# Kernel optimization log

Measured on AMD Instinct MI355X. Metric: run time of the kernel, lower is better.

## Reference

```python
import jax, jax.numpy as jnp
import numpy as np

S, IN, OUT = 2048, 512, 512
H, KV = 16, 4            # query heads, kv heads (cross-broadcast + averaged)
DQ = DK = DV = 64        # per-head embedding dims


def setup_inputs() -> dict:
    key = jax.random.key(0)
    ks = jax.random.split(key, 5)
    lim_in = 1.0 / np.sqrt(IN)
    lim_o = 1.0 / np.sqrt(H * DV)
    x = jax.random.normal(ks[0], (S, IN), dtype=jnp.float32)
    Wq = jax.random.uniform(ks[1], (H * DQ, IN), jnp.float32, -lim_in, lim_in)
    Wk = jax.random.uniform(ks[2], (KV * DK, IN), jnp.float32, -lim_in, lim_in)
    Wv = jax.random.uniform(ks[3], (KV * DV, IN), jnp.float32, -lim_in, lim_in)
    Wo = jax.random.uniform(ks[4], (OUT, H * DV), jnp.float32, -lim_o, lim_o)
    return {"x": x, "Wq": Wq, "Wk": Wk, "Wv": Wv, "Wo": Wo}


def reference(x, Wq, Wk, Wv, Wo):
    seq = x.shape[0]
    # projections (eqx.nn.Linear: y = W @ x, no bias)
    q = (x @ Wq.T).reshape(seq, H, DQ)    # [S, H, DQ]
    k = (x @ Wk.T).reshape(seq, KV, DK)   # [S, KV, DK]
    v = (x @ Wv.T).reshape(seq, KV, DV)   # [S, KV, DV]
    # cross-broadcast every kv head against every query head -> [KV, H, S, S]
    scores = jnp.einsum('shd,tkd->khst', q, k) / jnp.sqrt(jnp.asarray(DK, x.dtype))
    # NOTE: original applies causal mask whenever `mask is not None`; the
    # boolean flag is always passed, so masking is effectively always on.
    causal = jnp.tril(jnp.ones((seq, seq), dtype=bool))
    scores = jnp.where(causal, scores, -jnp.inf)
    w = jax.nn.softmax(scores, axis=-1)   # [KV, H, S, S]
    # attn @ V, then sum over kv heads and average by KV
    o = jnp.einsum('khst,tkd->shd', w, v) / KV  # [S, H, DV]
    return o.reshape(seq, H * DV) @ Wo.T        # [S, OUT]
```

## Files before the change

### kernel.cpp

```cpp
#include <hip/hip_runtime.h>
#include <hip/hip_bf16.h>

#define SEQ   2048
#define INF_  512
#define HQ    16
#define KVH   4
#define DH    64
#define NQ    (HQ*DH)
#define NKV   (KVH*DH)
#define OUTD  512

typedef short v8s __attribute__((ext_vector_type(8)));
typedef float v4f __attribute__((ext_vector_type(4)));

static __device__ __forceinline__ float bf2f(unsigned short u) {
    union { unsigned int i; float f; } c;
    c.i = ((unsigned int)u) << 16;
    return c.f;
}
static __device__ __forceinline__ unsigned short f2bf(float f) {
    union { float f; unsigned int i; } c; c.f = f;
    unsigned int lsb = (c.i >> 16) & 1u;
    c.i += 0x7fffu + lsb;
    return (unsigned short)(c.i >> 16);
}
static __device__ __forceinline__ unsigned int f2bf2(float lo, float hi) {
    union { __hip_bfloat162 h; unsigned int u; } c;
    c.h = __float22bfloat162_rn(make_float2(lo, hi));
    return c.u;
}
static __device__ __forceinline__ v8s pack8(v4f a, v4f b) {
    union { v8s s; uint4 u; } c;
    c.u = make_uint4(f2bf2(a[0], a[1]), f2bf2(a[2], a[3]),
                     f2bf2(b[0], b[1]), f2bf2(b[2], b[3]));
    return c.s;
}

static __device__ __forceinline__ void gll16(const void* g, void* l) {
    __builtin_amdgcn_global_load_lds(
        (const __attribute__((address_space(1))) void*)g,
        (__attribute__((address_space(3))) void*)l, 16, 0, 0);
}

static __device__ __forceinline__ void stage_tile(
    const unsigned short* __restrict__ src, int stride, int kb,
    unsigned short* ldsbase, int w, int lane)
{
#pragma unroll
    for (int i = 0; i < 2; i++) {
        const int rl = w * 16 + i * 8 + (lane >> 3);
        const int kc = ((lane & 7) ^ (rl & 7)) * 8;
        gll16(src + (size_t)rl * stride + kb + kc,
              ldsbase + (w * 16 + i * 8) * 64);
    }
}

#define QSCALE 0.180336880f

__global__ __launch_bounds__(256) void cast_all(
    const float* __restrict__ x,  const float* __restrict__ Wq,
    const float* __restrict__ Wk, const float* __restrict__ Wv,
    const float* __restrict__ Wo,
    unsigned short* __restrict__ xb,  unsigned short* __restrict__ Wqb,
    unsigned short* __restrict__ Wkb, unsigned short* __restrict__ Wvb,
    unsigned short* __restrict__ Wob)
{
    size_t i = ((size_t)blockIdx.x * 256 + threadIdx.x) * 8;
    const float* s; unsigned short* d; size_t off;
    if (i < 1048576)      { s = x;  d = xb;  off = i; }
    else if (i < 1572864) { s = Wq; d = Wqb; off = i - 1048576; }
    else if (i < 1703936) { s = Wk; d = Wkb; off = i - 1572864; }
    else if (i < 1835008) { s = Wv; d = Wvb; off = i - 1703936; }
    else                  { s = Wo; d = Wob; off = i - 1835008; }
    float4 a = *(const float4*)(s + off);
    float4 b = *(const float4*)(s + off + 4);
    *(uint4*)(d + off) = make_uint4(f2bf2(a.x, a.y), f2bf2(a.z, a.w),
                                    f2bf2(b.x, b.y), f2bf2(b.z, b.w));
}

__global__ __launch_bounds__(256, 4) void gemm_qkv(
    const unsigned short* __restrict__ xb,
    const unsigned short* __restrict__ Wqb,
    const unsigned short* __restrict__ Wkb,
    const unsigned short* __restrict__ Wvb,
    unsigned short* __restrict__ Qg,
    unsigned short* __restrict__ Kg,
    unsigned short* __restrict__ Vg)
{
    __shared__ unsigned short Asb[2][4096];
    __shared__ unsigned short Bsb[2][4096];

    const int m0 = blockIdx.x * 64;
    const int n0 = blockIdx.y * 64;

    const unsigned short* Bp; int role;
    if (n0 < NQ)            { Bp = Wqb + (size_t)n0 * INF_;              role = 0; }
    else if (n0 < NQ + NKV) { Bp = Wkb + (size_t)(n0 - NQ) * INF_;       role = 1; }
    else                    { Bp = Wvb + (size_t)(n0 - NQ - NKV) * INF_; role = 2; }

    const int tid = threadIdx.x;
    const int w = tid >> 6, lane = tid & 63;
    const int n = lane & 15, quad = lane >> 4;
    const int m7 = n & 7;
    const int r0w = (w & 1) * 32, c0w = (w >> 1) * 32;
    const unsigned short* Ap = xb + (size_t)m0 * INF_;

    v4f acc[2][2];
#pragma unroll
    for (int rt = 0; rt < 2; rt++)
#pragma unroll
        for (int ct = 0; ct < 2; ct++) acc[rt][ct] = (v4f){0.f,0.f,0.f,0.f};

    stage_tile(Ap, INF_, 0, &Asb[0][0], w, lane);
    stage_tile(Bp, INF_, 0, &Bsb[0][0], w, lane);

    for (int kb = 0; kb < INF_; kb += 64) {
        const int buf = (kb >> 6) & 1;
        __syncthreads();
        if (kb + 64 < INF_) {
            stage_tile(Ap, INF_, kb + 64, &Asb[buf ^ 1][0], w, lane);
            stage_tile(Bp, INF_, kb + 64, &Bsb[buf ^ 1][0], w, lane);
        }
#pragma unroll
        for (int kk = 0; kk < 2; kk++) {
            const int gs = ((kk * 4 + quad) ^ m7) * 8;
            v8s a0 = *(const v8s*)&Asb[buf][(r0w + n) * 64 + gs];
            v8s a1 = *(const v8s*)&Asb[buf][(r0w + 16 + n) * 64 + gs];
            v8s b0 = *(const v8s*)&Bsb[buf][(c0w + n) * 64 + gs];
            v8s b1 = *(const v8s*)&Bsb[buf][(c0w + 16 + n) * 64 + gs];
            acc[0][0] = __builtin_amdgcn_mfma_f32_16x16x32_bf16(a0, b0, acc[0][0], 0, 0, 0);
            acc[0][1] = __builtin_amdgcn_mfma_f32_16x16x32_bf16(a0, b1, acc[0][1], 0, 0, 0);
            acc[1][0] = __builtin_amdgcn_mfma_f32_16x16x32_bf16(a1, b0, acc[1][0], 0, 0, 0);
            acc[1][1] = __builtin_amdgcn_mfma_f32_16x16x32_bf16(a1, b1, acc[1][1], 0, 0, 0);
        }
    }

    const int t = m0 >> 6;
    if (role == 0) {
        unsigned short* base = Qg + ((size_t)(t * 16 + (n0 >> 6))) * 4096;
#pragma unroll
        for (int rt = 0; rt < 2; rt++)
#pragma unroll
            for (int ct = 0; ct < 2; ct++)
#pragma unroll
                for (int reg = 0; reg < 4; reg++) {
                    const int r = r0w + rt * 16 + quad * 4 + reg;
                    const int d = c0w + ct * 16 + n;
                    base[r * 64 + (((d >> 3) ^ (r & 7)) * 8) + (d & 7)] =
                        f2bf(acc[rt][ct][reg] * QSCALE);
                }
    } else if (role == 1) {
        const int g = (n0 - NQ) >> 6;
        unsigned short* base = Kg + ((size_t)(g * 32 + t)) * 4096;
#pragma unroll
        for (int rt = 0; rt < 2; rt++)
#pragma unroll
            for (int ct = 0; ct < 2; ct++)
#pragma unroll
                for (int reg = 0; reg < 4; reg++) {
                    const int r = r0w + rt * 16 + quad * 4 + reg;
                    const int d = c0w + ct * 16 + n;
                    base[r * 64 + (((d >> 3) ^ (r & 7)) * 8) + (d & 7)] =
                        f2bf(acc[rt][ct][reg]);
                }
    } else {
        const int g = (n0 - NQ - NKV) >> 6;
        unsigned short* base = Vg + ((size_t)(g * 32 + t)) * 4096;
#pragma unroll
        for (int rt = 0; rt < 2; rt++)
#pragma unroll
            for (int ct = 0; ct < 2; ct++) {
                const int jb_ = r0w + rt * 16 + quad * 4;
                const int d = c0w + ct * 16 + n;
                const int p = (jb_ & 32) + (((jb_ >> 2) & 3) * 8) + (((jb_ >> 4) & 1) * 4);
                *(uint2*)&base[d * 64 + (((p >> 3) ^ (d & 7)) * 8) + (p & 7)] =
                    make_uint2(f2bf2(acc[rt][ct][0], acc[rt][ct][1]),
                               f2bf2(acc[rt][ct][2], acc[rt][ct][3]));
            }
    }
}

__global__ __launch_bounds__(256, 4) void attn_mfma(
    const unsigned short* __restrict__ Qg,
    const unsigned short* __restrict__ Kg,
    const unsigned short* __restrict__ Vg,
    unsigned short* __restrict__ Oh)
{
    __shared__ unsigned short Ksb[2][4096];
    __shared__ unsigned short Vsb[2][4096];

    const int bx = blockIdx.x;
    const int h  = bx & 15;
    const int jj = (bx >> 4) & 15;
    const int g  = bx >> 8;
    const int jj2 = (jj + 8 * (g >> 1)) & 15;
    const int qi2 = (g & 1) ? (15 - jj2) : jj2;
    const int q0 = qi2 * 128;
    const int tid = threadIdx.x;
    const int w = tid >> 6, lane = tid & 63;
    const int n = lane & 15, quad = lane >> 4;
    const int r0 = w * 32;
    const int m7 = n & 7;
    const int ntile = 2 * qi2 + 2;

    {
        const size_t off = ((size_t)(g * 32)) * 4096 + w * 1024 + lane * 8;
        gll16(Kg + off,       &Ksb[0][w * 1024]);
        gll16(Kg + off + 512, &Ksb[0][w * 1024 + 512]);
        gll16(Vg + off,       &Vsb[0][w * 1024]);
        gll16(Vg + off + 512, &Vsb[0][w * 1024 + 512]);
    }

    v8s qf[2][2];
    {
        const unsigned short* tb =
            Qg + ((size_t)((2 * qi2 + (r0 >> 6)) * 16 + h)) * 4096 + (r0 & 63) * 64;
#pragma unroll
        for (int qt = 0; qt < 2; qt++) {
            const unsigned short* rp = tb + (qt * 16 + n) * 64;
            qf[qt][0] = *(const v8s*)(rp + (quad ^ m7) * 8);
            qf[qt][1] = *(const v8s*)(rp + ((quad + 4) ^ m7) * 8);
        }
    }

    v8s ones;
#pragma unroll
    for (int i = 0; i < 8; i++) ones[i] = (short)0x3F80;

    v4f Lacc[2];
    Lacc[0] = (v4f){0.f,0.f,0.f,0.f};
    Lacc[1] = (v4f){0.f,0.f,0.f,0.f};
    v4f Oacc[2][4];
#pragma unroll
    for (int qt = 0; qt < 2; qt++)
#pragma unroll
        for (int dt = 0; dt < 4; dt++) Oacc[qt][dt] = (v4f){0.f,0.f,0.f,0.f};
    const v4f z = (v4f){0.f,0.f,0.f,0.f};

    for (int tt = 0; tt < ntile; tt++) {
        const int buf = tt & 1;
        __syncthreads();
        if (tt + 1 < ntile) {
            const size_t off = ((size_t)(g * 32 + tt + 1)) * 4096 + w * 1024 + lane * 8;
            const int nb = buf ^ 1;
            gll16(Kg + off,       &Ksb[nb][w * 1024]);
            gll16(Kg + off + 512, &Ksb[nb][w * 1024 + 512]);
            gll16(Vg + off,       &Vsb[nb][w * 1024]);
            gll16(Vg + off + 512, &Vsb[nb][w * 1024 + 512]);
        }
        const int t0 = tt * 64;
        const bool do0 = (t0 <= q0 + r0 + 15);
        const bool do1 = (t0 <= q0 + r0 + 31);
        if (!do1) continue;

        const unsigned short* Kb = Ksb[buf];
        const unsigned short* Vb = Vsb[buf];

        v4f sc[2][4];
#pragma unroll
        for (int jt = 0; jt < 4; jt++) {
            const int kr = (jt * 16 + n) * 64;
            v8s kf0 = *(const v8s*)&Kb[kr + (quad ^ m7) * 8];
            v8s kf1 = *(const v8s*)&Kb[kr + ((quad + 4) ^ m7) * 8];
            if (do0) {
                v4f tq = __builtin_amdgcn_mfma_f32_16x16x32_bf16(kf0, qf[0][0], z, 0, 0, 0);
                sc[0][jt] = __builtin_amdgcn_mfma_f32_16x16x32_bf16(kf1, qf[0][1], tq, 0, 0, 0);
            }
            v4f t1 = __builtin_amdgcn_mfma_f32_16x16x32_bf16(kf0, qf[1][0], z, 0, 0, 0);
            sc[1][jt] = __builtin_amdgcn_mfma_f32_16x16x32_bf16(kf1, qf[1][1], t1, 0, 0, 0);
        }

#pragma unroll
        for (int qt = 0; qt < 2; qt++) {
            if (qt == 0 && !do0) continue;
            const int qg = q0 + r0 + qt * 16 + n;
            if (t0 + 63 > q0 + r0 + qt * 16) {
#pragma unroll
                for (int jt = 0; jt < 4; jt++) {
                    const int jg = t0 + jt * 16 + quad * 4;
#pragma unroll
                    for (int reg = 0; reg < 4; reg++)
                        sc[qt][jt][reg] = (jg + reg <= qg) ? sc[qt][jt][reg] : -INFINITY;
                }
            }
#pragma unroll
            for (int jt = 0; jt < 4; jt++)
#pragma unroll
                for (int reg = 0; reg < 4; reg++)
                    sc[qt][jt][reg] = __builtin_amdgcn_exp2f(sc[qt][jt][reg]);
        }

        v8s pf[2][2];
        if (do0) {
            pf[0][0] = pack8(sc[0][0], sc[0][1]);
            pf[0][1] = pack8(sc[0][2], sc[0][3]);
        }
        pf[1][0] = pack8(sc[1][0], sc[1][1]);
        pf[1][1] = pack8(sc[1][2], sc[1][3]);

        if (do0) {
            Lacc[0] = __builtin_amdgcn_mfma_f32_16x16x32_bf16(ones, pf[0][0], Lacc[0], 0, 0, 0);
            Lacc[0] = __builtin_amdgcn_mfma_f32_16x16x32_bf16(ones, pf[0][1], Lacc[0], 0, 0, 0);
        }
        Lacc[1] = __builtin_amdgcn_mfma_f32_16x16x32_bf16(ones, pf[1][0], Lacc[1], 0, 0, 0);
        Lacc[1] = __builtin_amdgcn_mfma_f32_16x16x32_bf16(ones, pf[1][1], Lacc[1], 0, 0, 0);

#pragma unroll
        for (int dt = 0; dt < 4; dt++) {
            const int vr = (dt * 16 + n) * 64;
            v8s vf0 = *(const v8s*)&Vb[vr + (quad ^ m7) * 8];
            v8s vf1 = *(const v8s*)&Vb[vr + ((quad + 4) ^ m7) * 8];
            if (do0) {
                Oacc[0][dt] = __builtin_amdgcn_mfma_f32_16x16x32_bf16(vf0, pf[0][0], Oacc[0][dt], 0, 0, 0);
                Oacc[0][dt] = __builtin_amdgcn_mfma_f32_16x16x32_bf16(vf1, pf[0][1], Oacc[0][dt], 0, 0, 0);
            }
            Oacc[1][dt] = __builtin_amdgcn_mfma_f32_16x16x32_bf16(vf0, pf[1][0], Oacc[1][dt], 0, 0, 0);
            Oacc[1][dt] = __builtin_amdgcn_mfma_f32_16x16x32_bf16(vf1, pf[1][1], Oacc[1][dt], 0, 0, 0);
        }
    }

    unsigned short* Ohp = Oh + (size_t)g * ((size_t)SEQ * NQ);
#pragma unroll
    for (int qt = 0; qt < 2; qt++) {
        const float inv = 0.25f / Lacc[qt][0];
        const int row = q0 + r0 + qt * 16 + n;
        unsigned short* dst = Ohp + (size_t)row * NQ + h * DH + quad * 4;
#pragma unroll
        for (int dt = 0; dt < 4; dt++) {
            uint2 pk = make_uint2(f2bf2(Oacc[qt][dt][0] * inv, Oacc[qt][dt][1] * inv),
                                  f2bf2(Oacc[qt][dt][2] * inv, Oacc[qt][dt][3] * inv));
            *(uint2*)(dst + dt * 16) = pk;
        }
    }
}

__global__ __launch_bounds__(256, 4) void gemm_out(
    const unsigned short* __restrict__ Oh,
    const unsigned short* __restrict__ Wob,
    float* __restrict__ C)
{
    __shared__ unsigned short Asb[32][72];
    __shared__ unsigned short Bsb[64][72];

    const int m0 = blockIdx.x * 32;
    const int n0 = blockIdx.y * 64;
    const int tid = threadIdx.x;
    const int w = tid >> 6, lane = tid & 63;
    const int n = lane & 15, quad = lane >> 4;
    const int rw = (w & 1) * 16, cw = (w >> 1) * 32;
    const int ar = tid >> 3, akc = (tid & 7) * 8;
    const int br = tid >> 2, bkc = (tid & 3) * 16;

    v4f acc[2];
    acc[0] = (v4f){0.f,0.f,0.f,0.f};
    acc[1] = (v4f){0.f,0.f,0.f,0.f};

    const size_t plane = (size_t)SEQ * NQ;
    const size_t abase = (size_t)(m0 + ar) * NQ + akc;
    const unsigned short* bp = Wob + (size_t)(n0 + br) * NQ + bkc;

    uint4 ua[4];
#pragma unroll
    for (int g = 0; g < 4; g++) ua[g] = *(const uint4*)(Oh + g * plane + abase);
    uint4 ub0 = *(const uint4*)(bp), ub1 = *(const uint4*)(bp + 8);

    for (int kb = 0; kb < NQ; kb += 64) {
        __syncthreads();
        {
            unsigned int ow[4];
#pragma unroll
            for (int q = 0; q < 4; q++) {
                const unsigned int u0 = ((const unsigned int*)&ua[0])[q];
                const unsigned int u1 = ((const unsigned int*)&ua[1])[q];
                const unsigned int u2 = ((const unsigned int*)&ua[2])[q];
                const unsigned int u3 = ((const unsigned int*)&ua[3])[q];
                float lo = bf2f((unsigned short)(u0 & 0xffffu)) + bf2f((unsigned short)(u1 & 0xffffu))
                         + bf2f((unsigned short)(u2 & 0xffffu)) + bf2f((unsigned short)(u3 & 0xffffu));
                float hi = bf2f((unsigned short)(u0 >> 16)) + bf2f((unsigned short)(u1 >> 16))
                         + bf2f((unsigned short)(u2 >> 16)) + bf2f((unsigned short)(u3 >> 16));
                ow[q] = f2bf2(lo, hi);
            }
            *(uint4*)&Asb[ar][akc] = make_uint4(ow[0], ow[1], ow[2], ow[3]);
        }
        *(uint4*)&Bsb[br][bkc]     = ub0;
        *(uint4*)&Bsb[br][bkc + 8] = ub1;
        __syncthreads();
        if (kb + 64 < NQ) {
#pragma unroll
            for (int g = 0; g < 4; g++)
                ua[g] = *(const uint4*)(Oh + g * plane + abase + kb + 64);
            ub0 = *(const uint4*)(bp + kb + 64);
            ub1 = *(const uint4*)(bp + kb + 64 + 8);
        }
#pragma unroll
        for (int kk = 0; kk < 2; kk++) {
            v8s a  = *(const v8s*)&Asb[rw + n][kk * 32 + quad * 8];
            v8s b0 = *(const v8s*)&Bsb[cw + n][kk * 32 + quad * 8];
            v8s b1 = *(const v8s*)&Bsb[cw + 16 + n][kk * 32 + quad * 8];
            acc[0] = __builtin_amdgcn_mfma_f32_16x16x32_bf16(a, b0, acc[0], 0, 0, 0);
            acc[1] = __builtin_amdgcn_mfma_f32_16x16x32_bf16(a, b1, acc[1], 0, 0, 0);
        }
    }

#pragma unroll
    for (int ct = 0; ct < 2; ct++)
#pragma unroll
        for (int reg = 0; reg < 4; reg++) {
            const int row = m0 + rw + quad * 4 + reg;
            const int col = n0 + cw + ct * 16 + n;
            C[(size_t)row * OUTD + col] = acc[ct][reg];
        }
}

extern "C" void kernel_launch(void* const* d_in, const int* in_sizes, int n_in,
                              void* d_out, int out_size, void* d_ws, size_t ws_size,
                              hipStream_t stream) {
    const float* x  = (const float*)d_in[0];
    const float* Wq = (const float*)d_in[1];
    const float* Wk = (const float*)d_in[2];
    const float* Wv = (const float*)d_in[3];
    const float* Wo = (const float*)d_in[4];
    float* out = (float*)d_out;

    char* base = (char*)d_ws;
    unsigned short* Oh  = (unsigned short*)(base);
    unsigned short* xb  = (unsigned short*)(base);
    unsigned short* Wqb = (unsigned short*)(base + 2097152);
    unsigned short* Wkb = (unsigned short*)(base + 3145728);
    unsigned short* Wvb = (unsigned short*)(base + 3407872);
    unsigned short* Qg  = (unsigned short*)(base + 16777216);
    unsigned short* Kg  = (unsigned short*)(base + 20971520);
    unsigned short* Vg  = (unsigned short*)(base + 22020096);
    unsigned short* Wob = (unsigned short*)(base + 23068672);

    dim3 blk(256);
    cast_all<<<dim3(1152), blk, 0, stream>>>(x, Wq, Wk, Wv, Wo,
                                             xb, Wqb, Wkb, Wvb, Wob);
    gemm_qkv<<<dim3(SEQ / 64, (NQ + 2 * NKV) / 64), blk, 0, stream>>>(
        xb, Wqb, Wkb, Wvb, Qg, Kg, Vg);
    attn_mfma<<<dim3(1024), blk, 0, stream>>>(Qg, Kg, Vg, Oh);
    gemm_out<<<dim3(SEQ / 32, OUTD / 64), blk, 0, stream>>>(Oh, Wob, out);
}
```

Before: 142.0 us.

## Fuse fp32-to-bf16 casts into GEMMs and read K/V tiles directly from global

```diff
diff --git a/kernel.cpp b/kernel.cpp
--- a/kernel.cpp
+++ b/kernel.cpp
@@ -36,74 +36,33 @@
     return c.s;
 }
 
-static __device__ __forceinline__ void gll16(const void* g, void* l) {
-    __builtin_amdgcn_global_load_lds(
-        (const __attribute__((address_space(1))) void*)g,
-        (__attribute__((address_space(3))) void*)l, 16, 0, 0);
-}
-
-static __device__ __forceinline__ void stage_tile(
-    const unsigned short* __restrict__ src, int stride, int kb,
-    unsigned short* ldsbase, int w, int lane)
-{
-#pragma unroll
-    for (int i = 0; i < 2; i++) {
-        const int rl = w * 16 + i * 8 + (lane >> 3);
-        const int kc = ((lane & 7) ^ (rl & 7)) * 8;
-        gll16(src + (size_t)rl * stride + kb + kc,
-              ldsbase + (w * 16 + i * 8) * 64);
-    }
-}
-
 #define QSCALE 0.180336880f
 
-__global__ __launch_bounds__(256) void cast_all(
-    const float* __restrict__ x,  const float* __restrict__ Wq,
-    const float* __restrict__ Wk, const float* __restrict__ Wv,
-    const float* __restrict__ Wo,
-    unsigned short* __restrict__ xb,  unsigned short* __restrict__ Wqb,
-    unsigned short* __restrict__ Wkb, unsigned short* __restrict__ Wvb,
-    unsigned short* __restrict__ Wob)
-{
-    size_t i = ((size_t)blockIdx.x * 256 + threadIdx.x) * 8;
-    const float* s; unsigned short* d; size_t off;
-    if (i < 1048576)      { s = x;  d = xb;  off = i; }
-    else if (i < 1572864) { s = Wq; d = Wqb; off = i - 1048576; }
-    else if (i < 1703936) { s = Wk; d = Wkb; off = i - 1572864; }
-    else if (i < 1835008) { s = Wv; d = Wvb; off = i - 1703936; }
-    else                  { s = Wo; d = Wob; off = i - 1835008; }
-    float4 a = *(const float4*)(s + off);
-    float4 b = *(const float4*)(s + off + 4);
-    *(uint4*)(d + off) = make_uint4(f2bf2(a.x, a.y), f2bf2(a.z, a.w),
-                                    f2bf2(b.x, b.y), f2bf2(b.z, b.w));
-}
-
 __global__ __launch_bounds__(256, 4) void gemm_qkv(
-    const unsigned short* __restrict__ xb,
-    const unsigned short* __restrict__ Wqb,
-    const unsigned short* __restrict__ Wkb,
-    const unsigned short* __restrict__ Wvb,
+    const float* __restrict__ x,
+    const float* __restrict__ Wq,
+    const float* __restrict__ Wk,
+    const float* __restrict__ Wv,
     unsigned short* __restrict__ Qg,
     unsigned short* __restrict__ Kg,
     unsigned short* __restrict__ Vg)
 {
-    __shared__ unsigned short Asb[2][4096];
-    __shared__ unsigned short Bsb[2][4096];
+    __shared__ unsigned short Asb[64][72];
+    __shared__ unsigned short Bsb[64][72];
 
     const int m0 = blockIdx.x * 64;
     const int n0 = blockIdx.y * 64;
 
-    const unsigned short* Bp; int role;
-    if (n0 < NQ)            { Bp = Wqb + (size_t)n0 * INF_;              role = 0; }
-    else if (n0 < NQ + NKV) { Bp = Wkb + (size_t)(n0 - NQ) * INF_;       role = 1; }
-    else                    { Bp = Wvb + (size_t)(n0 - NQ - NKV) * INF_; role = 2; }
+    const float* Bp; int role;
+    if (n0 < NQ)            { Bp = Wq + (size_t)n0 * INF_;              role = 0; }
+    else if (n0 < NQ + NKV) { Bp = Wk + (size_t)(n0 - NQ) * INF_;       role = 1; }
+    else                    { Bp = Wv + (size_t)(n0 - NQ - NKV) * INF_; role = 2; }
 
     const int tid = threadIdx.x;
     const int w = tid >> 6, lane = tid & 63;
     const int n = lane & 15, quad = lane >> 4;
-    const int m7 = n & 7;
     const int r0w = (w & 1) * 32, c0w = (w >> 1) * 32;
-    const unsigned short* Ap = xb + (size_t)m0 * INF_;
+    const int sr = tid >> 2, skc = (tid & 3) * 16;
 
     v4f acc[2][2];
 #pragma unroll
@@ -111,23 +70,40 @@
 #pragma unroll
         for (int ct = 0; ct < 2; ct++) acc[rt][ct] = (v4f){0.f,0.f,0.f,0.f};
 
-    stage_tile(Ap, INF_, 0, &Asb[0][0], w, lane);
-    stage_tile(Bp, INF_, 0, &Bsb[0][0], w, lane);
+    const float* ap = x  + (size_t)(m0 + sr) * INF_ + skc;
+    const float* bp = Bp + (size_t)sr * INF_ + skc;
+
+    float4 pa[4], pb[4];
+#pragma unroll
+    for (int i = 0; i < 4; i++) {
+        pa[i] = *(const float4*)(ap + 4 * i);
+        pb[i] = *(const float4*)(bp + 4 * i);
+    }
 
     for (int kb = 0; kb < INF_; kb += 64) {
-        const int buf = (kb >> 6) & 1;
+        __syncthreads();
+        *(uint4*)&Asb[sr][skc]     = make_uint4(f2bf2(pa[0].x,pa[0].y), f2bf2(pa[0].z,pa[0].w),
+                                                f2bf2(pa[1].x,pa[1].y), f2bf2(pa[1].z,pa[1].w));
+        *(uint4*)&Asb[sr][skc + 8] = make_uint4(f2bf2(pa[2].x,pa[2].y), f2bf2(pa[2].z,pa[2].w),
+                                                f2bf2(pa[3].x,pa[3].y), f2bf2(pa[3].z,pa[3].w));
+        *(uint4*)&Bsb[sr][skc]     = make_uint4(f2bf2(pb[0].x,pb[0].y), f2bf2(pb[0].z,pb[0].w),
+                                                f2bf2(pb[1].x,pb[1].y), f2bf2(pb[1].z,pb[1].w));
+        *(uint4*)&Bsb[sr][skc + 8] = make_uint4(f2bf2(pb[2].x,pb[2].y), f2bf2(pb[2].z,pb[2].w),
+                                                f2bf2(pb[3].x,pb[3].y), f2bf2(pb[3].z,pb[3].w));
         __syncthreads();
         if (kb + 64 < INF_) {
-            stage_tile(Ap, INF_, kb + 64, &Asb[buf ^ 1][0], w, lane);
-            stage_tile(Bp, INF_, kb + 64, &Bsb[buf ^ 1][0], w, lane);
+#pragma unroll
+            for (int i = 0; i < 4; i++) {
+                pa[i] = *(const float4*)(ap + kb + 64 + 4 * i);
+                pb[i] = *(const float4*)(bp + kb + 64 + 4 * i);
+            }
         }
 #pragma unroll
         for (int kk = 0; kk < 2; kk++) {
-            const int gs = ((kk * 4 + quad) ^ m7) * 8;
-            v8s a0 = *(const v8s*)&Asb[buf][(r0w + n) * 64 + gs];
-            v8s a1 = *(const v8s*)&Asb[buf][(r0w + 16 + n) * 64 + gs];
-            v8s b0 = *(const v8s*)&Bsb[buf][(c0w + n) * 64 + gs];
-            v8s b1 = *(const v8s*)&Bsb[buf][(c0w + 16 + n) * 64 + gs];
+            v8s a0 = *(const v8s*)&Asb[r0w + n][kk * 32 + quad * 8];
+            v8s a1 = *(const v8s*)&Asb[r0w + 16 + n][kk * 32 + quad * 8];
+            v8s b0 = *(const v8s*)&Bsb[c0w + n][kk * 32 + quad * 8];
+            v8s b1 = *(const v8s*)&Bsb[c0w + 16 + n][kk * 32 + quad * 8];
             acc[0][0] = __builtin_amdgcn_mfma_f32_16x16x32_bf16(a0, b0, acc[0][0], 0, 0, 0);
             acc[0][1] = __builtin_amdgcn_mfma_f32_16x16x32_bf16(a0, b1, acc[0][1], 0, 0, 0);
             acc[1][0] = __builtin_amdgcn_mfma_f32_16x16x32_bf16(a1, b0, acc[1][0], 0, 0, 0);
@@ -186,9 +162,6 @@
     const unsigned short* __restrict__ Vg,
     unsigned short* __restrict__ Oh)
 {
-    __shared__ unsigned short Ksb[2][4096];
-    __shared__ unsigned short Vsb[2][4096];
-
     const int bx = blockIdx.x;
     const int h  = bx & 15;
     const int jj = (bx >> 4) & 15;
@@ -201,15 +174,12 @@
     const int n = lane & 15, quad = lane >> 4;
     const int r0 = w * 32;
     const int m7 = n & 7;
-    const int ntile = 2 * qi2 + 2;
-
-    {
-        const size_t off = ((size_t)(g * 32)) * 4096 + w * 1024 + lane * 8;
-        gll16(Kg + off,       &Ksb[0][w * 1024]);
-        gll16(Kg + off + 512, &Ksb[0][w * 1024 + 512]);
-        gll16(Vg + off,       &Vsb[0][w * 1024]);
-        gll16(Vg + off + 512, &Vsb[0][w * 1024 + 512]);
-    }
+    const int ntw = ((q0 + r0 + 31) >> 6) + 1;
+
+    int off[4];
+#pragma unroll
+    for (int t4 = 0; t4 < 4; t4++)
+        off[t4] = (t4 * 16 + n) * 64 + ((quad ^ m7) * 8);
 
     v8s qf[2][2];
     {
@@ -237,42 +207,27 @@
         for (int dt = 0; dt < 4; dt++) Oacc[qt][dt] = (v4f){0.f,0.f,0.f,0.f};
     const v4f z = (v4f){0.f,0.f,0.f,0.f};
 
-    for (int tt = 0; tt < ntile; tt++) {
-        const int buf = tt & 1;
-        __syncthreads();
-        if (tt + 1 < ntile) {
-            const size_t off = ((size_t)(g * 32 + tt + 1)) * 4096 + w * 1024 + lane * 8;
-            const int nb = buf ^ 1;
-            gll16(Kg + off,       &Ksb[nb][w * 1024]);
-            gll16(Kg + off + 512, &Ksb[nb][w * 1024 + 512]);
-            gll16(Vg + off,       &Vsb[nb][w * 1024]);
-            gll16(Vg + off + 512, &Vsb[nb][w * 1024 + 512]);
-        }
+    const unsigned short* Ktile = Kg + ((size_t)(g * 32)) * 4096;
+    const unsigned short* Vtile = Vg + ((size_t)(g * 32)) * 4096;
+
+    for (int tt = 0; tt < ntw; tt++) {
+        const unsigned short* Kt = Ktile + (size_t)tt * 4096;
+        const unsigned short* Vt = Vtile + (size_t)tt * 4096;
         const int t0 = tt * 64;
-        const bool do0 = (t0 <= q0 + r0 + 15);
-        const bool do1 = (t0 <= q0 + r0 + 31);
-        if (!do1) continue;
-
-        const unsigned short* Kb = Ksb[buf];
-        const unsigned short* Vb = Vsb[buf];
 
         v4f sc[2][4];
 #pragma unroll
         for (int jt = 0; jt < 4; jt++) {
-            const int kr = (jt * 16 + n) * 64;
-            v8s kf0 = *(const v8s*)&Kb[kr + (quad ^ m7) * 8];
-            v8s kf1 = *(const v8s*)&Kb[kr + ((quad + 4) ^ m7) * 8];
-            if (do0) {
-                v4f tq = __builtin_amdgcn_mfma_f32_16x16x32_bf16(kf0, qf[0][0], z, 0, 0, 0);
-                sc[0][jt] = __builtin_amdgcn_mfma_f32_16x16x32_bf16(kf1, qf[0][1], tq, 0, 0, 0);
-            }
+            v8s kf0 = *(const v8s*)(Kt + off[jt]);
+            v8s kf1 = *(const v8s*)(Kt + (off[jt] ^ 32));
+            v4f tq = __builtin_amdgcn_mfma_f32_16x16x32_bf16(kf0, qf[0][0], z, 0, 0, 0);
+            sc[0][jt] = __builtin_amdgcn_mfma_f32_16x16x32_bf16(kf1, qf[0][1], tq, 0, 0, 0);
             v4f t1 = __builtin_amdgcn_mfma_f32_16x16x32_bf16(kf0, qf[1][0], z, 0, 0, 0);
             sc[1][jt] = __builtin_amdgcn_mfma_f32_16x16x32_bf16(kf1, qf[1][1], t1, 0, 0, 0);
         }
 
 #pragma unroll
         for (int qt = 0; qt < 2; qt++) {
-            if (qt == 0 && !do0) continue;
             const int qg = q0 + r0 + qt * 16 + n;
             if (t0 + 63 > q0 + r0 + qt * 16) {
 #pragma unroll
@@ -291,29 +246,22 @@
         }
 
         v8s pf[2][2];
-        if (do0) {
-            pf[0][0] = pack8(sc[0][0], sc[0][1]);
-            pf[0][1] = pack8(sc[0][2], sc[0][3]);
-        }
+        pf[0][0] = pack8(sc[0][0], sc[0][1]);
+        pf[0][1] = pack8(sc[0][2], sc[0][3]);
         pf[1][0] = pack8(sc[1][0], sc[1][1]);
         pf[1][1] = pack8(sc[1][2], sc[1][3]);
 
-        if (do0) {
-            Lacc[0] = __builtin_amdgcn_mfma_f32_16x16x32_bf16(ones, pf[0][0], Lacc[0], 0, 0, 0);
-            Lacc[0] = __builtin_amdgcn_mfma_f32_16x16x32_bf16(ones, pf[0][1], Lacc[0], 0, 0, 0);
-        }
+        Lacc[0] = __builtin_amdgcn_mfma_f32_16x16x32_bf16(ones, pf[0][0], Lacc[0], 0, 0, 0);
+        Lacc[0] = __builtin_amdgcn_mfma_f32_16x16x32_bf16(ones, pf[0][1], Lacc[0], 0, 0, 0);
         Lacc[1] = __builtin_amdgcn_mfma_f32_16x16x32_bf16(ones, pf[1][0], Lacc[1], 0, 0, 0);
         Lacc[1] = __builtin_amdgcn_mfma_f32_16x16x32_bf16(ones, pf[1][1], Lacc[1], 0, 0, 0);
 
 #pragma unroll
         for (int dt = 0; dt < 4; dt++) {
-            const int vr = (dt * 16 + n) * 64;
-            v8s vf0 = *(const v8s*)&Vb[vr + (quad ^ m7) * 8];
-            v8s vf1 = *(const v8s*)&Vb[vr + ((quad + 4) ^ m7) * 8];
-            if (do0) {
-                Oacc[0][dt] = __builtin_amdgcn_mfma_f32_16x16x32_bf16(vf0, pf[0][0], Oacc[0][dt], 0, 0, 0);
-                Oacc[0][dt] = __builtin_amdgcn_mfma_f32_16x16x32_bf16(vf1, pf[0][1], Oacc[0][dt], 0, 0, 0);
-            }
+            v8s vf0 = *(const v8s*)(Vt + off[dt]);
+            v8s vf1 = *(const v8s*)(Vt + (off[dt] ^ 32));
+            Oacc[0][dt] = __builtin_amdgcn_mfma_f32_16x16x32_bf16(vf0, pf[0][0], Oacc[0][dt], 0, 0, 0);
+            Oacc[0][dt] = __builtin_amdgcn_mfma_f32_16x16x32_bf16(vf1, pf[0][1], Oacc[0][dt], 0, 0, 0);
             Oacc[1][dt] = __builtin_amdgcn_mfma_f32_16x16x32_bf16(vf0, pf[1][0], Oacc[1][dt], 0, 0, 0);
             Oacc[1][dt] = __builtin_amdgcn_mfma_f32_16x16x32_bf16(vf1, pf[1][1], Oacc[1][dt], 0, 0, 0);
         }
@@ -336,7 +284,7 @@
 
 __global__ __launch_bounds__(256, 4) void gemm_out(
     const unsigned short* __restrict__ Oh,
-    const unsigned short* __restrict__ Wob,
+    const float* __restrict__ Wo,
     float* __restrict__ C)
 {
     __shared__ unsigned short Asb[32][72];
@@ -357,12 +305,14 @@
 
     const size_t plane = (size_t)SEQ * NQ;
     const size_t abase = (size_t)(m0 + ar) * NQ + akc;
-    const unsigned short* bp = Wob + (size_t)(n0 + br) * NQ + bkc;
+    const float* bp = Wo + (size_t)(n0 + br) * NQ + bkc;
 
     uint4 ua[4];
 #pragma unroll
     for (int g = 0; g < 4; g++) ua[g] = *(const uint4*)(Oh + g * plane + abase);
-    uint4 ub0 = *(const uint4*)(bp), ub1 = *(const uint4*)(bp + 8);
+    float4 pb[4];
+#pragma unroll
+    for (int i = 0; i < 4; i++) pb[i] = *(const float4*)(bp + 4 * i);
 
     for (int kb = 0; kb < NQ; kb += 64) {
         __syncthreads();
@@ -382,15 +332,17 @@
             }
             *(uint4*)&Asb[ar][akc] = make_uint4(ow[0], ow[1], ow[2], ow[3]);
         }
-        *(uint4*)&Bsb[br][bkc]     = ub0;
-        *(uint4*)&Bsb[br][bkc + 8] = ub1;
+        *(uint4*)&Bsb[br][bkc]     = make_uint4(f2bf2(pb[0].x,pb[0].y), f2bf2(pb[0].z,pb[0].w),
+                                                f2bf2(pb[1].x,pb[1].y), f2bf2(pb[1].z,pb[1].w));
+        *(uint4*)&Bsb[br][bkc + 8] = make_uint4(f2bf2(pb[2].x,pb[2].y), f2bf2(pb[2].z,pb[2].w),
+                                                f2bf2(pb[3].x,pb[3].y), f2bf2(pb[3].z,pb[3].w));
         __syncthreads();
         if (kb + 64 < NQ) {
 #pragma unroll
             for (int g = 0; g < 4; g++)
                 ua[g] = *(const uint4*)(Oh + g * plane + abase + kb + 64);
-            ub0 = *(const uint4*)(bp + kb + 64);
-            ub1 = *(const uint4*)(bp + kb + 64 + 8);
+#pragma unroll
+            for (int i = 0; i < 4; i++) pb[i] = *(const float4*)(bp + kb + 64 + 4 * i);
         }
 #pragma unroll
         for (int kk = 0; kk < 2; kk++) {
@@ -423,21 +375,14 @@
     float* out = (float*)d_out;
 
     char* base = (char*)d_ws;
-    unsigned short* Oh  = (unsigned short*)(base);
-    unsigned short* xb  = (unsigned short*)(base);
-    unsigned short* Wqb = (unsigned short*)(base + 2097152);
-    unsigned short* Wkb = (unsigned short*)(base + 3145728);
-    unsigned short* Wvb = (unsigned short*)(base + 3407872);
-    unsigned short* Qg  = (unsigned short*)(base + 16777216);
-    unsigned short* Kg  = (unsigned short*)(base + 20971520);
-    unsigned short* Vg  = (unsigned short*)(base + 22020096);
-    unsigned short* Wob = (unsigned short*)(base + 23068672);
+    unsigned short* Oh = (unsigned short*)(base);
+    unsigned short* Qg = (unsigned short*)(base + 16777216);
+    unsigned short* Kg = (unsigned short*)(base + 20971520);
+    unsigned short* Vg = (unsigned short*)(base + 22020096);
 
     dim3 blk(256);
-    cast_all<<<dim3(1152), blk, 0, stream>>>(x, Wq, Wk, Wv, Wo,
-                                             xb, Wqb, Wkb, Wvb, Wob);
     gemm_qkv<<<dim3(SEQ / 64, (NQ + 2 * NKV) / 64), blk, 0, stream>>>(
-        xb, Wqb, Wkb, Wvb, Qg, Kg, Vg);
+        x, Wq, Wk, Wv, Qg, Kg, Vg);
     attn_mfma<<<dim3(1024), blk, 0, stream>>>(Qg, Kg, Vg, Oh);
-    gemm_out<<<dim3(SEQ / 32, OUTD / 64), blk, 0, stream>>>(Oh, Wob, out);
-}
+    gemm_out<<<dim3(SEQ / 32, OUTD / 64), blk, 0, stream>>>(Oh, Wo, out);
+}
```

Result: slower. 197.7 us (+39.2%).
